# Performance work log

Hardware: AMD Instinct MI355X
Metric: run time of the kernel (lower is better)

## Reference

```python
import jax, jax.numpy as jnp
import numpy as np

N_TOKENS = 1_000_000
NUM_FEATURES = 128
NUM_CLUSTERS = 64


def setup_inputs() -> dict:
    key = jax.random.key(0)
    kx, kc = jax.random.split(key)
    x = jax.random.normal(kx, (1, N_TOKENS, NUM_FEATURES), dtype=jnp.float32)
    # learned parameter, initialized as torch.randn(num_clusters, num_features)
    cluster_centers = jax.random.normal(kc, (NUM_CLUSTERS, NUM_FEATURES), dtype=jnp.float32)
    return {"x": x, "cluster_centers": cluster_centers}


def reference(x, cluster_centers):
    # x: (1, n, d); cluster_centers: (k, d)
    # O(n*k*d) broadcast intermediate of the original). argmin is identical
    # to argmin over torch.norm since sqrt is monotone.
    x2 = jnp.sum(x * x, axis=-1)                                  # (1, n)
    c2 = jnp.sum(cluster_centers * cluster_centers, axis=-1)      # (k,)
    xc = jnp.einsum('bnd,kd->bnk', x, cluster_centers)            # (1, n, k)
    d2 = x2[..., None] + c2[None, None, :] - 2.0 * xc             # (1, n, k)
    # nearest token index for each cluster (min over the token dim)
    indices = jnp.argmin(d2, axis=1)                              # (1, k)
    # gather the selected token features: (1, k, d)
    selected = x[:, indices[0], :]
    return selected
```

## Files before the change

kernel.cpp:

```cpp
#include <hip/hip_runtime.h>
#include <math.h>

#define NTOK   1000000
#define NFEAT  128
#define NCLUS  64
#define TT     64
#define NTILES (NTOK / TT)
#define GRID_A 512

__global__ __launch_bounds__(256, 2)
void cluster_part_kernel(const float* __restrict__ x, const float* __restrict__ cc,
                         float* __restrict__ pv, int* __restrict__ pi)
{
    __shared__ float cs[NFEAT][NCLUS];
    __shared__ float xs[NFEAT][TT];

    const int tid  = threadIdx.x;
    const int tx   = tid & 15;
    const int ty   = tid >> 4;
    const int lsub = tid & 3;
    const int row  = tid >> 2;

    float c2part = 0.f;
    {
        const float* src = cc + row * NFEAT;
        #pragma unroll
        for (int r = 0; r < 8; ++r) {
            int f = (lsub + 4 * r) * 4;
            float4 v = *(const float4*)(src + f);
            cs[f + 0][row] = v.x; cs[f + 1][row] = v.y;
            cs[f + 2][row] = v.z; cs[f + 3][row] = v.w;
            c2part = fmaf(v.x, v.x, c2part);
            c2part = fmaf(v.y, v.y, c2part);
            c2part = fmaf(v.z, v.z, c2part);
            c2part = fmaf(v.w, v.w, c2part);
        }
        c2part += __shfl_xor(c2part, 1);
        c2part += __shfl_xor(c2part, 2);
    }
    if (lsub == 0) xs[0][row] = c2part;
    __syncthreads();
    float c2r[4];
    #pragma unroll
    for (int j = 0; j < 4; ++j) c2r[j] = xs[0][tx * 4 + j];

    float bestv[4]; int besti[4];
    #pragma unroll
    for (int j = 0; j < 4; ++j) { bestv[j] = INFINITY; besti[j] = 0; }

    for (int tile = blockIdx.x; tile < NTILES; tile += GRID_A) {
        __syncthreads();
        float x2tot;
        {
            const float* src = x + (size_t)(tile * TT + row) * NFEAT;
            float s = 0.f;
            #pragma unroll
            for (int r = 0; r < 8; ++r) {
                int f = (lsub + 4 * r) * 4;
                float4 v = *(const float4*)(src + f);
                xs[f + 0][row] = v.x; xs[f + 1][row] = v.y;
                xs[f + 2][row] = v.z; xs[f + 3][row] = v.w;
                s = fmaf(v.x, v.x, s);
                s = fmaf(v.y, v.y, s);
                s = fmaf(v.z, v.z, s);
                s = fmaf(v.w, v.w, s);
            }
            s += __shfl_xor(s, 1);
            s += __shfl_xor(s, 2);
            x2tot = s;
        }
        __syncthreads();

        float x2r[4];
        #pragma unroll
        for (int i = 0; i < 4; ++i)
            x2r[i] = __shfl(x2tot, ((ty & 3) * 4 + i) * 4, 64);

        float acc[4][4];
        #pragma unroll
        for (int i = 0; i < 4; ++i)
            #pragma unroll
            for (int j = 0; j < 4; ++j) acc[i][j] = 0.f;

        #pragma unroll 8
        for (int k = 0; k < NFEAT; ++k) {
            float4 xv = *(const float4*)&xs[k][ty * 4];
            float4 cv = *(const float4*)&cs[k][tx * 4];
            acc[0][0] = fmaf(xv.x, cv.x, acc[0][0]);
            acc[0][1] = fmaf(xv.x, cv.y, acc[0][1]);
            acc[0][2] = fmaf(xv.x, cv.z, acc[0][2]);
            acc[0][3] = fmaf(xv.x, cv.w, acc[0][3]);
            acc[1][0] = fmaf(xv.y, cv.x, acc[1][0]);
            acc[1][1] = fmaf(xv.y, cv.y, acc[1][1]);
            acc[1][2] = fmaf(xv.y, cv.z, acc[1][2]);
            acc[1][3] = fmaf(xv.y, cv.w, acc[1][3]);
            acc[2][0] = fmaf(xv.z, cv.x, acc[2][0]);
            acc[2][1] = fmaf(xv.z, cv.y, acc[2][1]);
            acc[2][2] = fmaf(xv.z, cv.z, acc[2][2]);
            acc[2][3] = fmaf(xv.z, cv.w, acc[2][3]);
            acc[3][0] = fmaf(xv.w, cv.x, acc[3][0]);
            acc[3][1] = fmaf(xv.w, cv.y, acc[3][1]);
            acc[3][2] = fmaf(xv.w, cv.z, acc[3][2]);
            acc[3][3] = fmaf(xv.w, cv.w, acc[3][3]);
        }

        const int nbase = tile * TT + ty * 4;
        #pragma unroll
        for (int i = 0; i < 4; ++i) {
            #pragma unroll
            for (int j = 0; j < 4; ++j) {
                float s = (x2r[i] + c2r[j]) - 2.0f * acc[i][j];
                if (s < bestv[j]) { bestv[j] = s; besti[j] = nbase + i; }
            }
        }
    }

    __syncthreads();
    float* rv = &xs[0][0];
    int*   ri = (int*)&cs[0][0];
    #pragma unroll
    for (int j = 0; j < 4; ++j) {
        rv[(tx * 4 + j) * 16 + ty] = bestv[j];
        ri[(tx * 4 + j) * 16 + ty] = besti[j];
    }
    __syncthreads();
    if (tid < NCLUS) {
        float bv = rv[tid * 16]; int bi = ri[tid * 16];
        #pragma unroll
        for (int t = 1; t < 16; ++t) {
            float v = rv[tid * 16 + t]; int ii = ri[tid * 16 + t];
            if (v < bv || (v == bv && ii < bi)) { bv = v; bi = ii; }
        }
        pv[blockIdx.x * NCLUS + tid] = bv;
        pi[blockIdx.x * NCLUS + tid] = bi;
    }
}

__global__ __launch_bounds__(256)
void cluster_final_kernel(const float* __restrict__ x,
                          const float* __restrict__ pv, const int* __restrict__ pi,
                          float* __restrict__ out)
{
    const int c   = blockIdx.x;
    const int tid = threadIdx.x;
    __shared__ float sv[256];
    __shared__ int   si[256];

    float bv = INFINITY; int bi = 0;
    for (int b = tid; b < GRID_A; b += 256) {
        float v = pv[b * NCLUS + c]; int ii = pi[b * NCLUS + c];
        if (v < bv || (v == bv && ii < bi)) { bv = v; bi = ii; }
    }
    sv[tid] = bv; si[tid] = bi;
    __syncthreads();
    for (int s = 128; s > 0; s >>= 1) {
        if (tid < s) {
            float v = sv[tid + s]; int ii = si[tid + s];
            if (v < sv[tid] || (v == sv[tid] && ii < si[tid])) {
                sv[tid] = v; si[tid] = ii;
            }
        }
        __syncthreads();
    }
    const int best = si[0];
    if (tid < NFEAT) out[c * NFEAT + tid] = x[(size_t)best * NFEAT + tid];
}

extern "C" void kernel_launch(void* const* d_in, const int* in_sizes, int n_in,
                              void* d_out, int out_size, void* d_ws, size_t ws_size,
                              hipStream_t stream) {
    const float* x  = (const float*)d_in[0];
    const float* cc = (const float*)d_in[1];
    float* out = (float*)d_out;

    float* pv = (float*)d_ws;
    int*   pi = (int*)((char*)d_ws + (size_t)GRID_A * NCLUS * sizeof(float));

    cluster_part_kernel<<<GRID_A, 256, 0, stream>>>(x, cc, pv, pi);
    cluster_final_kernel<<<NCLUS, 256, 0, stream>>>(x, pv, pi, out);
}
```

Baseline: 758.0 us.

## Use one 256-token tile per block with 8x8 register tiles and K-chunked LDS

```diff
diff --git a/kernel.cpp b/kernel.cpp
--- a/kernel.cpp
+++ b/kernel.cpp
@@ -4,114 +4,112 @@
 #define NTOK   1000000
 #define NFEAT  128
 #define NCLUS  64
-#define TT     64
-#define NTILES (NTOK / TT)
-#define GRID_A 512
+#define TT     256
+#define KC     32
+#define XPAD   260
+#define NTILES ((NTOK + TT - 1) / TT)
 
-__global__ __launch_bounds__(256, 2)
+__global__ __launch_bounds__(256, 3)
 void cluster_part_kernel(const float* __restrict__ x, const float* __restrict__ cc,
                          float* __restrict__ pv, int* __restrict__ pi)
 {
-    __shared__ float cs[NFEAT][NCLUS];
-    __shared__ float xs[NFEAT][TT];
+    __shared__ float xs[KC][XPAD];
+    __shared__ float cs[KC][NCLUS];
+    __shared__ float x2s[TT];
+    __shared__ float c2s[NCLUS];
 
-    const int tid  = threadIdx.x;
-    const int tx   = tid & 15;
-    const int ty   = tid >> 4;
-    const int lsub = tid & 3;
-    const int row  = tid >> 2;
+    const int tid = threadIdx.x;
+    const int cg  = tid & 7;
+    const int tg  = tid >> 3;
+    const int l   = tid & 3;
+    const int g   = tid >> 2;
 
-    float c2part = 0.f;
-    {
-        const float* src = cc + row * NFEAT;
+    const int  tile = blockIdx.x;
+    const long tb   = (long)tile * TT;
+
+    float acc[8][8];
+    #pragma unroll
+    for (int i = 0; i < 8; ++i)
         #pragma unroll
-        for (int r = 0; r < 8; ++r) {
-            int f = (lsub + 4 * r) * 4;
-            float4 v = *(const float4*)(src + f);
-            cs[f + 0][row] = v.x; cs[f + 1][row] = v.y;
-            cs[f + 2][row] = v.z; cs[f + 3][row] = v.w;
-            c2part = fmaf(v.x, v.x, c2part);
-            c2part = fmaf(v.y, v.y, c2part);
-            c2part = fmaf(v.z, v.z, c2part);
-            c2part = fmaf(v.w, v.w, c2part);
-        }
-        c2part += __shfl_xor(c2part, 1);
-        c2part += __shfl_xor(c2part, 2);
-    }
-    if (lsub == 0) xs[0][row] = c2part;
-    __syncthreads();
-    float c2r[4];
-    #pragma unroll
-    for (int j = 0; j < 4; ++j) c2r[j] = xs[0][tx * 4 + j];
+        for (int j = 0; j < 8; ++j) acc[i][j] = 0.f;
 
-    float bestv[4]; int besti[4];
-    #pragma unroll
-    for (int j = 0; j < 4; ++j) { bestv[j] = INFINITY; besti[j] = 0; }
+    for (int kc = 0; kc < NFEAT / KC; ++kc) {
+        __syncthreads();
 
-    for (int tile = blockIdx.x; tile < NTILES; tile += GRID_A) {
-        __syncthreads();
-        float x2tot;
         {
-            const float* src = x + (size_t)(tile * TT + row) * NFEAT;
+            const float* src = cc + (long)g * NFEAT + kc * KC + l * 4;
+            float4 a = *(const float4*)(src);
+            float4 b = *(const float4*)(src + 16);
+            cs[l*4+0][g] = a.x; cs[l*4+1][g] = a.y;
+            cs[l*4+2][g] = a.z; cs[l*4+3][g] = a.w;
+            cs[16+l*4+0][g] = b.x; cs[16+l*4+1][g] = b.y;
+            cs[16+l*4+2][g] = b.z; cs[16+l*4+3][g] = b.w;
             float s = 0.f;
-            #pragma unroll
-            for (int r = 0; r < 8; ++r) {
-                int f = (lsub + 4 * r) * 4;
-                float4 v = *(const float4*)(src + f);
-                xs[f + 0][row] = v.x; xs[f + 1][row] = v.y;
-                xs[f + 2][row] = v.z; xs[f + 3][row] = v.w;
-                s = fmaf(v.x, v.x, s);
-                s = fmaf(v.y, v.y, s);
-                s = fmaf(v.z, v.z, s);
-                s = fmaf(v.w, v.w, s);
-            }
+            s = fmaf(a.x, a.x, s); s = fmaf(a.y, a.y, s);
+            s = fmaf(a.z, a.z, s); s = fmaf(a.w, a.w, s);
+            s = fmaf(b.x, b.x, s); s = fmaf(b.y, b.y, s);
+            s = fmaf(b.z, b.z, s); s = fmaf(b.w, b.w, s);
             s += __shfl_xor(s, 1);
             s += __shfl_xor(s, 2);
-            x2tot = s;
+            if (l == 0) { if (kc == 0) c2s[g] = s; else c2s[g] += s; }
+        }
+
+        #pragma unroll
+        for (int r = 0; r < 4; ++r) {
+            const int  row = r * 64 + g;
+            long n = tb + row;
+            if (n > NTOK - 1) n = NTOK - 1;
+            const float* src = x + n * NFEAT + kc * KC + l * 4;
+            float4 a = *(const float4*)(src);
+            float4 b = *(const float4*)(src + 16);
+            xs[l*4+0][row] = a.x; xs[l*4+1][row] = a.y;
+            xs[l*4+2][row] = a.z; xs[l*4+3][row] = a.w;
+            xs[16+l*4+0][row] = b.x; xs[16+l*4+1][row] = b.y;
+            xs[16+l*4+2][row] = b.z; xs[16+l*4+3][row] = b.w;
+            float s = 0.f;
+            s = fmaf(a.x, a.x, s); s = fmaf(a.y, a.y, s);
+            s = fmaf(a.z, a.z, s); s = fmaf(a.w, a.w, s);
+            s = fmaf(b.x, b.x, s); s = fmaf(b.y, b.y, s);
+            s = fmaf(b.z, b.z, s); s = fmaf(b.w, b.w, s);
+            s += __shfl_xor(s, 1);
+            s += __shfl_xor(s, 2);
+            if (l == 0) { if (kc == 0) x2s[row] = s; else x2s[row] += s; }
         }
         __syncthreads();
 
-        float x2r[4];
+        #pragma unroll 2
+        for (int k = 0; k < KC; ++k) {
+            float4 xa = *(const float4*)&xs[k][tg * 8];
+            float4 xb = *(const float4*)&xs[k][tg * 8 + 4];
+            float4 ca = *(const float4*)&cs[k][cg * 8];
+            float4 cb = *(const float4*)&cs[k][cg * 8 + 4];
+            float xv[8] = {xa.x, xa.y, xa.z, xa.w, xb.x, xb.y, xb.z, xb.w};
+            float cv[8] = {ca.x, ca.y, ca.z, ca.w, cb.x, cb.y, cb.z, cb.w};
+            #pragma unroll
+            for (int i = 0; i < 8; ++i)
+                #pragma unroll
+                for (int j = 0; j < 8; ++j)
+                    acc[i][j] = fmaf(xv[i], cv[j], acc[i][j]);
+        }
+    }
+
+    float bestv[8]; int besti[8];
+    #pragma unroll
+    for (int j = 0; j < 8; ++j) { bestv[j] = INFINITY; besti[j] = 0; }
+
+    float c2r[8];
+    #pragma unroll
+    for (int j = 0; j < 8; ++j) c2r[j] = c2s[cg * 8 + j];
+
+    #pragma unroll
+    for (int i = 0; i < 8; ++i) {
+        const long n = tb + tg * 8 + i;
+        if (n >= NTOK) continue;
+        const float x2 = x2s[tg * 8 + i];
         #pragma unroll
-        for (int i = 0; i < 4; ++i)
-            x2r[i] = __shfl(x2tot, ((ty & 3) * 4 + i) * 4, 64);
-
-        float acc[4][4];
-        #pragma unroll
-        for (int i = 0; i < 4; ++i)
-            #pragma unroll
-            for (int j = 0; j < 4; ++j) acc[i][j] = 0.f;
-
-        #pragma unroll 8
-        for (int k = 0; k < NFEAT; ++k) {
-            float4 xv = *(const float4*)&xs[k][ty * 4];
-            float4 cv = *(const float4*)&cs[k][tx * 4];
-            acc[0][0] = fmaf(xv.x, cv.x, acc[0][0]);
-            acc[0][1] = fmaf(xv.x, cv.y, acc[0][1]);
-            acc[0][2] = fmaf(xv.x, cv.z, acc[0][2]);
-            acc[0][3] = fmaf(xv.x, cv.w, acc[0][3]);
-            acc[1][0] = fmaf(xv.y, cv.x, acc[1][0]);
-            acc[1][1] = fmaf(xv.y, cv.y, acc[1][1]);
-            acc[1][2] = fmaf(xv.y, cv.z, acc[1][2]);
-            acc[1][3] = fmaf(xv.y, cv.w, acc[1][3]);
-            acc[2][0] = fmaf(xv.z, cv.x, acc[2][0]);
-            acc[2][1] = fmaf(xv.z, cv.y, acc[2][1]);
-            acc[2][2] = fmaf(xv.z, cv.z, acc[2][2]);
-            acc[2][3] = fmaf(xv.z, cv.w, acc[2][3]);
-            acc[3][0] = fmaf(xv.w, cv.x, acc[3][0]);
-            acc[3][1] = fmaf(xv.w, cv.y, acc[3][1]);
-            acc[3][2] = fmaf(xv.w, cv.z, acc[3][2]);
-            acc[3][3] = fmaf(xv.w, cv.w, acc[3][3]);
-        }
-
-        const int nbase = tile * TT + ty * 4;
-        #pragma unroll
-        for (int i = 0; i < 4; ++i) {
-            #pragma unroll
-            for (int j = 0; j < 4; ++j) {
-                float s = (x2r[i] + c2r[j]) - 2.0f * acc[i][j];
-                if (s < bestv[j]) { bestv[j] = s; besti[j] = nbase + i; }
-            }
+        for (int j = 0; j < 8; ++j) {
+            float s = (x2 + c2r[j]) - 2.0f * acc[i][j];
+            if (s < bestv[j]) { bestv[j] = s; besti[j] = (int)n; }
         }
     }
 
@@ -119,20 +117,20 @@
     float* rv = &xs[0][0];
     int*   ri = (int*)&cs[0][0];
     #pragma unroll
-    for (int j = 0; j < 4; ++j) {
-        rv[(tx * 4 + j) * 16 + ty] = bestv[j];
-        ri[(tx * 4 + j) * 16 + ty] = besti[j];
+    for (int j = 0; j < 8; ++j) {
+        rv[(cg * 8 + j) * 32 + tg] = bestv[j];
+        ri[(cg * 8 + j) * 32 + tg] = besti[j];
     }
     __syncthreads();
     if (tid < NCLUS) {
-        float bv = rv[tid * 16]; int bi = ri[tid * 16];
+        float bv = rv[tid * 32]; int bi = ri[tid * 32];
         #pragma unroll
-        for (int t = 1; t < 16; ++t) {
-            float v = rv[tid * 16 + t]; int ii = ri[tid * 16 + t];
+        for (int t = 1; t < 32; ++t) {
+            float v = rv[tid * 32 + t]; int ii = ri[tid * 32 + t];
             if (v < bv || (v == bv && ii < bi)) { bv = v; bi = ii; }
         }
-        pv[blockIdx.x * NCLUS + tid] = bv;
-        pi[blockIdx.x * NCLUS + tid] = bi;
+        pv[(long)tile * NCLUS + tid] = bv;
+        pi[(long)tile * NCLUS + tid] = bi;
     }
 }
 
@@ -146,9 +144,9 @@
     __shared__ float sv[256];
     __shared__ int   si[256];
 
-    float bv = INFINITY; int bi = 0;
-    for (int b = tid; b < GRID_A; b += 256) {
-        float v = pv[b * NCLUS + c]; int ii = pi[b * NCLUS + c];
+    float bv = INFINITY; int bi = 0x7fffffff;
+    for (int b = tid; b < NTILES; b += 256) {
+        float v = pv[(long)b * NCLUS + c]; int ii = pi[(long)b * NCLUS + c];
         if (v < bv || (v == bv && ii < bi)) { bv = v; bi = ii; }
     }
     sv[tid] = bv; si[tid] = bi;
@@ -163,7 +161,7 @@
         __syncthreads();
     }
     const int best = si[0];
-    if (tid < NFEAT) out[c * NFEAT + tid] = x[(size_t)best * NFEAT + tid];
+    if (tid < NFEAT) out[c * NFEAT + tid] = x[(long)best * NFEAT + tid];
 }
 
 extern "C" void kernel_launch(void* const* d_in, const int* in_sizes, int n_in,
@@ -174,8 +172,8 @@
     float* out = (float*)d_out;
 
     float* pv = (float*)d_ws;
-    int*   pi = (int*)((char*)d_ws + (size_t)GRID_A * NCLUS * sizeof(float));
+    int*   pi = (int*)((char*)d_ws + (size_t)NTILES * NCLUS * sizeof(float));
 
-    cluster_part_kernel<<<GRID_A, 256, 0, stream>>>(x, cc, pv, pi);
+    cluster_part_kernel<<<NTILES, 256, 0, stream>>>(x, cc, pv, pi);
     cluster_final_kernel<<<NCLUS, 256, 0, stream>>>(x, pv, pi, out);
 }
```

Result: slower. 778.7 us (+2.7%).
